# Optimization experiments

Measured on AMD Instinct MI355X. Metric: run time of the kernel, lower is better.

Reference implementation:

```python
import jax, jax.numpy as jnp
import numpy as np

H = 768          # hidden_size
HH = H // 2      # 384


def setup_inputs() -> dict:
    key = jax.random.key(0)
    ks = jax.random.split(key, 16)
    B, W, E, R = 32, 512, 128, 1024
    inp = {
        "hidden_states": jax.random.normal(ks[0], (B, W, H), dtype=jnp.float32),
        "relation_head": jax.random.randint(ks[1], (B, R), 0, E),
        "relation_tail": jax.random.randint(ks[2], (B, R), 0, E),
        "relation_label": jax.random.randint(ks[3], (B, R), 0, 2),
        "entities_start": jax.random.randint(ks[4], (B, E), 0, W),
        "entities_end": jax.random.randint(ks[5], (B, E), 0, W),
        "entities_label": jax.random.randint(ks[6], (B, E), 0, 3),
        # parameters (torch Linear convention: weight [out, in])
        "entity_emb": jax.random.normal(ks[7], (3, H), dtype=jnp.float32) * 0.02,
        "Wh1": jax.random.normal(ks[8], (H, 2 * H), dtype=jnp.float32) * 0.02,
        "bh1": jnp.zeros((H,), jnp.float32),
        "Wh2": jax.random.normal(ks[9], (HH, H), dtype=jnp.float32) * 0.02,
        "bh2": jnp.zeros((HH,), jnp.float32),
        "Wt1": jax.random.normal(ks[10], (H, 2 * H), dtype=jnp.float32) * 0.02,
        "bt1": jnp.zeros((H,), jnp.float32),
        "Wt2": jax.random.normal(ks[11], (HH, H), dtype=jnp.float32) * 0.02,
        "bt2": jnp.zeros((HH,), jnp.float32),
        "W_bil": jax.random.normal(ks[12], (2, HH, HH), dtype=jnp.float32) * 0.02,
        "W_lin": jax.random.normal(ks[13], (2, 2 * HH), dtype=jnp.float32) * 0.02,
        "b_lin": jnp.zeros((2,), jnp.float32),
    }
    return inp


def _ffnn(x, W1, b1, W2, b2):
    # two-layer MLP with ReLU (dropout is identity in eval mode)
    h = jax.nn.relu(jnp.einsum('brd,hd->brh', x, W1) + b1)
    return jax.nn.relu(jnp.einsum('brh,oh->bro', h, W2) + b2)


def reference(hidden_states, relation_head, relation_tail, relation_label,
              entities_start, entities_end, entities_label,
              entity_emb, Wh1, bh1, Wh2, bh2, Wt1, bt1, Wt2, bt2,
              W_bil, W_lin, b_lin):
    # gather per-relation entity info: [B, R]
    head_index = jnp.take_along_axis(entities_start, relation_head, axis=1)
    head_label = jnp.take_along_axis(entities_label, relation_head, axis=1)
    tail_index = jnp.take_along_axis(entities_start, relation_tail, axis=1)
    tail_label = jnp.take_along_axis(entities_label, relation_tail, axis=1)

    # gather token reprs: [B, R, H]
    head_tok = jnp.take_along_axis(hidden_states, head_index[:, :, None], axis=1)
    tail_tok = jnp.take_along_axis(hidden_states, tail_index[:, :, None], axis=1)

    head_repr = jnp.concatenate([head_tok, entity_emb[head_label]], axis=-1)  # [B,R,2H]
    tail_repr = jnp.concatenate([tail_tok, entity_emb[tail_label]], axis=-1)

    heads = _ffnn(head_repr, Wh1, bh1, Wh2, bh2)  # [B,R,HH]
    tails = _ffnn(tail_repr, Wt1, bt1, Wt2, bt2)

    # biaffine: bilinear + linear on concat
    bil = jnp.einsum('bri,oij,brj->bro', heads, W_bil, tails)
    lin = jnp.einsum('brc,oc->bro', jnp.concatenate([heads, tails], axis=-1), W_lin) + b_lin
    logits = bil + lin  # [B, R, 2]

    # per-doc mean CE summed over docs
    logp = jax.nn.log_softmax(logits, axis=-1)
    nll = -jnp.take_along_axis(logp, relation_label[:, :, None], axis=-1)[..., 0]  # [B,R]
    loss = jnp.sum(jnp.mean(nll, axis=1))
    return loss
```

## Files before the change

### kernel.cpp

```cpp
#include <hip/hip_runtime.h>
#include <math.h>

typedef unsigned short u16;
typedef __bf16 bf16x8 __attribute__((ext_vector_type(8)));
typedef float f32x4 __attribute__((ext_vector_type(4)));

#define B_ 32
#define W_ 512
#define H_ 768
#define HH_ 384
#define E_ 128
#define R_ 1024
#define BE_ (B_*E_)
#define K1_ (2*H_)
#define BKK 64

__device__ __forceinline__ u16 f2bf(float f) {
  unsigned u = __float_as_uint(f);
  u = (u + 0x7fffu + ((u >> 16) & 1u)) >> 16;
  return (u16)u;
}
__device__ __forceinline__ float bf2f(u16 u) {
  return __uint_as_float(((unsigned)u) << 16);
}

__device__ __forceinline__ void gload_lds16(const void* g, void* l) {
  __builtin_amdgcn_global_load_lds(
      (__attribute__((address_space(1))) void*)(g),
      (__attribute__((address_space(3))) void*)(l), 16, 0, 0);
}

__device__ __forceinline__ void xcd_swizzle(int& bx, int& by) {
  const int nwg = gridDim.x * gridDim.y;
  int orig = blockIdx.y * gridDim.x + blockIdx.x;
  int q = nwg >> 3, r = nwg & 7;
  int xcd = orig & 7, idx = orig >> 3;
  int wgid = (xcd < r ? xcd * (q + 1) : r * (q + 1) + (xcd - r) * q) + idx;
  bx = wgid % gridDim.x;
  by = wgid / gridDim.x;
}

#define NBLK_W 2017
#define NBLK_P 1152
#define NBLK_X 4096

__global__ __launch_bounds__(256) void prep_all(
    const float* __restrict__ Wh1, const float* __restrict__ Wt1,
    const float* __restrict__ Wh2, const float* __restrict__ Wt2,
    const float* __restrict__ Wbil,
    const float* __restrict__ bh1, const float* __restrict__ bt1,
    const float* __restrict__ bh2, const float* __restrict__ bt2,
    const float* __restrict__ emb,
    const float* __restrict__ hs, const int* __restrict__ ent_start,
    u16* __restrict__ W1c, u16* __restrict__ W2c, u16* __restrict__ Wb,
    float* __restrict__ b2cat, float* __restrict__ P, u16* __restrict__ X)
{
  const int blk = blockIdx.x;
  const int tid = threadIdx.x;

  if (blk < NBLK_W) {
    const int i = blk * 256 + tid;
    const int SW1 = 294912;
    const int SW2 = SW1 + 147456;
    const int SWB = SW2 + 73728;
    const int SB2 = SWB + 192;
    if (i < SW1) {
      int row = i / 192, c = i % 192;
      const float4* src = (const float4*)((row < 768)
          ? (Wh1 + (size_t)row * K1_) : (Wt1 + (size_t)(row - 768) * K1_));
      float4 v = src[c];
      ushort4 o; o.x = f2bf(v.x); o.y = f2bf(v.y); o.z = f2bf(v.z); o.w = f2bf(v.w);
      ((ushort4*)W1c)[i] = o;
    } else if (i < SW2) {
      int j = i - SW1;
      float4 v = (j < 73728) ? ((const float4*)Wh2)[j]
                             : ((const float4*)Wt2)[j - 73728];
      ushort4 o; o.x = f2bf(v.x); o.y = f2bf(v.y); o.z = f2bf(v.z); o.w = f2bf(v.w);
      ((ushort4*)W2c)[j] = o;
    } else if (i < SWB) {
      int j = i - SW2;
      float4 v = ((const float4*)Wbil)[j];
      ushort4 o; o.x = f2bf(v.x); o.y = f2bf(v.y); o.z = f2bf(v.z); o.w = f2bf(v.w);
      ((ushort4*)Wb)[j] = o;
    } else if (i < SB2) {
      int j = i - SWB;
      ((float4*)b2cat)[j] = (j < 96) ? ((const float4*)bh2)[j]
                                     : ((const float4*)bt2)[j - 96];
    }
  } else if (blk < NBLK_W + NBLK_P) {
    const int w = (blk - NBLK_W) * 4 + (tid >> 6);
    const int lane = tid & 63;
    const int l = w / K1_;
    const int n = w - l * K1_;
    const float* wrow = (n < 768) ? (Wh1 + (size_t)n * K1_ + 768)
                                  : (Wt1 + (size_t)(n - 768) * K1_ + 768);
    const float  bb   = (n < 768) ? bh1[n] : bt1[n - 768];
    const float* ev = emb + (size_t)l * H_;
    float s = 0.f;
#pragma unroll
    for (int t = 0; t < 12; ++t) {
      int d = lane + 64 * t;
      s += ev[d] * wrow[d];
    }
#pragma unroll
    for (int off = 32; off; off >>= 1) s += __shfl_down(s, off);
    if (lane == 0) P[(size_t)l * K1_ + n] = s + bb;
  } else {
    const int be = blk - (NBLK_W + NBLK_P);
    if (tid < 192) {
      int b = be >> 7;
      int start = ent_start[be];
      const float4* s0 = (const float4*)(hs + ((size_t)b * W_ + start) * H_);
      float4 v = s0[tid];
      ushort4 o; o.x = f2bf(v.x); o.y = f2bf(v.y); o.z = f2bf(v.z); o.w = f2bf(v.w);
      ((ushort4*)(X + (size_t)be * H_))[tid] = o;
    }
  }
}

#define BM 128
#define BN 128

__global__ __launch_bounds__(256, 2) void gemm_bf16(
    const u16* __restrict__ A, int lda,
    const u16* __restrict__ Wt,
    const float* __restrict__ bias,
    u16* __restrict__ C, int ldc,
    int M, int N, int K, int do_relu, int half_n, int aoff,
    const float* __restrict__ rowBias,
    const int* __restrict__ rowLabel, int ldP)
{
  __shared__ char smem[2 * 32768];

  int bx, by;
  xcd_swizzle(bx, by);
  const int bn = bx * BN;
  const int bm = by * BM;

  const int tid  = threadIdx.x;
  const int wid  = tid >> 6;
  const int lane = tid & 63;
  const int wm = ((wid >> 1) & 1) * 64;
  const int wn = (wid & 1) * 64;

  const int a0 = (half_n && bn >= half_n) ? aoff : 0;

  const int srow = lane >> 3;
  const int sk8  = (lane & 7) ^ srow;
  const u16* gA = A  + (size_t)(bm + 32*wid + srow) * lda + a0 + 8*sk8;
  const u16* gB = Wt + (size_t)(bn + 32*wid + srow) * K  + 8*sk8;

  const int frow = lane & 15;
  const int fk8  = lane >> 4;

  f32x4 acc[4][4] = {};

  auto stage = [&](int buf, int k0) {
    char* As = smem + buf * 32768;
    char* Bs = As + 16384;
#pragma unroll
    for (int i = 0; i < 4; ++i) {
      gload_lds16(gA + k0 + (size_t)i * 8 * lda, As + (4*wid + i) * 1024);
      gload_lds16(gB + k0 + (size_t)i * 8 * K,   Bs + (4*wid + i) * 1024);
    }
  };

  const int nt = K / BKK;
  stage(0, 0);

  for (int t = 0; t < nt; ++t) {
    const int cur = t & 1;
    if (t + 1 < nt) {
      stage(cur ^ 1, (t + 1) * BKK);
      asm volatile("s_waitcnt vmcnt(8)" ::: "memory");
    } else {
      asm volatile("s_waitcnt vmcnt(0)" ::: "memory");
    }
    __builtin_amdgcn_s_barrier();

    char* As = smem + cur * 32768;
    char* Bs = As + 16384;
#pragma unroll
    for (int kh = 0; kh < 2; ++kh) {
      bf16x8 a[4], b[4];
#pragma unroll
      for (int m = 0; m < 4; ++m) {
        const int row  = wm + m*16 + frow;
        const int slot = (kh*4 + fk8) ^ (row & 7);
        a[m] = *(const bf16x8*)(As + row*128 + slot*16);
      }
#pragma unroll
      for (int n = 0; n < 4; ++n) {
        const int row  = wn + n*16 + frow;
        const int slot = (kh*4 + fk8) ^ (row & 7);
        b[n] = *(const bf16x8*)(Bs + row*128 + slot*16);
      }
#pragma unroll
      for (int m = 0; m < 4; ++m)
#pragma unroll
        for (int n = 0; n < 4; ++n)
          acc[m][n] = __builtin_amdgcn_mfma_f32_16x16x32_bf16(
              a[m], b[n], acc[m][n], 0, 0, 0);
    }

    if (t + 1 < nt)
      __builtin_amdgcn_s_barrier();
  }

  int lbl[4][4];
  if (rowLabel) {
#pragma unroll
    for (int m = 0; m < 4; ++m)
#pragma unroll
      for (int r = 0; r < 4; ++r)
        lbl[m][r] = rowLabel[bm + wm + m*16 + fk8*4 + r];
  }

#pragma unroll
  for (int n = 0; n < 4; ++n) {
    const int col = bn + wn + n*16 + frow;
    const float bv = bias ? bias[col] : 0.f;
    float p0 = 0.f, p1 = 0.f, p2 = 0.f;
    if (rowLabel) {
      p0 = rowBias[col];
      p1 = rowBias[ldP + col];
      p2 = rowBias[2*ldP + col];
    }
#pragma unroll
    for (int m = 0; m < 4; ++m) {
#pragma unroll
      for (int r = 0; r < 4; ++r) {
        const int row = bm + wm + m*16 + fk8*4 + r;
        float v = acc[m][n][r] + bv;
        if (rowLabel) {
          int l = lbl[m][r];
          v += (l == 0) ? p0 : ((l == 1) ? p1 : p2);
        }
        if (do_relu) v = fmaxf(v, 0.f);
        C[(size_t)row * ldc + col] = f2bf(v);
      }
    }
  }
}

__global__ __launch_bounds__(256, 2) void gemm_S_ce(
    const u16* __restrict__ Hcat, const u16* __restrict__ U,
    const float* __restrict__ linHT, const float* __restrict__ b_lin,
    const int* __restrict__ rel_head, const int* __restrict__ rel_tail,
    const int* __restrict__ rel_label, float* __restrict__ out)
{
  __shared__ char smem[2 * 16384];
  __shared__ float Sl[64][65];
  __shared__ float red[4];

  const int xcd = blockIdx.x & 7, idx = blockIdx.x >> 3;
  const int wgid = xcd * 32 + idx;
  const int bn = (wgid & 3) * 64;
  const int zz = wgid >> 2;
  const int z  = zz >> 1;
  const int bm = (zz & 1) * 64;

  const int tid  = threadIdx.x;
  const int wid  = tid >> 6;
  const int lane = tid & 63;
  const int srow = lane >> 3;
  const int sk8  = (lane & 7) ^ srow;

  auto stage = [&](int buf, int k0) {
    char* base = smem + buf * 16384;
#pragma unroll
    for (int i = 0; i < 4; ++i) {
      const int u = wid * 4 + i;
      if (u < 8) {
        const int row = z*128 + bm + u*8 + srow;
        gload_lds16(Hcat + (size_t)row * 768 + k0 + 8*sk8, base + u*1024);
      } else {
        const int row = bn + (u - 8)*8 + srow;
        gload_lds16(U + (size_t)z*98304 + (size_t)row * 384 + k0 + 8*sk8,
                    base + u*1024);
      }
    }
  };

  const int wm = (wid >> 1) * 32;
  const int wn = (wid & 1) * 32;
  const int frow = lane & 15;
  const int fk8  = lane >> 4;

  f32x4 acc[2][2] = {};

  stage(0, 0);

  for (int t = 0; t < 6; ++t) {
    const int cur = t & 1;
    if (t + 1 < 6) {
      stage(cur ^ 1, (t + 1) * BKK);
      asm volatile("s_waitcnt vmcnt(4)" ::: "memory");
    } else {
      asm volatile("s_waitcnt vmcnt(0)" ::: "memory");
    }
    __builtin_amdgcn_s_barrier();

    char* As = smem + cur * 16384;
    char* Bs = As + 8192;
#pragma unroll
    for (int kh = 0; kh < 2; ++kh) {
      bf16x8 a[2], b[2];
#pragma unroll
      for (int m = 0; m < 2; ++m) {
        const int row  = wm + m*16 + frow;
        const int slot = (kh*4 + fk8) ^ (row & 7);
        a[m] = *(const bf16x8*)(As + row*128 + slot*16);
      }
#pragma unroll
      for (int n = 0; n < 2; ++n) {
        const int row  = wn + n*16 + frow;
        const int slot = (kh*4 + fk8) ^ (row & 7);
        b[n] = *(const bf16x8*)(Bs + row*128 + slot*16);
      }
#pragma unroll
      for (int m = 0; m < 2; ++m)
#pragma unroll
        for (int n = 0; n < 2; ++n)
          acc[m][n] = __builtin_amdgcn_mfma_f32_16x16x32_bf16(
              a[m], b[n], acc[m][n], 0, 0, 0);
    }

    if (t + 1 < 6)
      __builtin_amdgcn_s_barrier();
  }

  const int o = frow & 1;
  const float blv = b_lin[o];
#pragma unroll
  for (int n = 0; n < 2; ++n) {
    const int lc = wn + n*16 + frow;
    const int e2 = (bn + lc) >> 1;
    const float lt = linHT[(size_t)(z*128 + e2) * 4 + 2 + o];
#pragma unroll
    for (int m = 0; m < 2; ++m) {
#pragma unroll
      for (int r = 0; r < 4; ++r) {
        const int lr = wm + m*16 + fk8*4 + r;
        const float lh = linHT[(size_t)(z*128 + bm + lr) * 4 + o];
        Sl[lr][lc] = acc[m][n][r] + lh + lt + blv;
      }
    }
  }
  __syncthreads();

  float nllsum = 0.f;
#pragma unroll
  for (int j = 0; j < 4; ++j) {
    const int i = z * 1024 + tid + 256 * j;
    const int rh = rel_head[i];
    const int rt = rel_tail[i];
    const int lab = rel_label[i];
    if ((unsigned)(rh - bm) < 64u && (unsigned)(rt*2 - bn) < 64u) {
      const float l0 = Sl[rh - bm][rt*2 - bn];
      const float l1 = Sl[rh - bm][rt*2 - bn + 1];
      const float mx = fmaxf(l0, l1);
      const float lse = mx + logf(expf(l0 - mx) + expf(l1 - mx));
      nllsum += lse - (lab == 0 ? l0 : l1);
    }
  }
#pragma unroll
  for (int off = 32; off; off >>= 1) nllsum += __shfl_down(nllsum, off);
  if (lane == 0) red[wid] = nllsum;
  __syncthreads();
  if (tid == 0)
    atomicAdd(out, (red[0] + red[1] + red[2] + red[3]) * (1.0f / R_));
}

__global__ __launch_bounds__(256) void lin_parts_kernel(
    const u16* __restrict__ Hcat, const float* __restrict__ W_lin,
    float* __restrict__ linHT, float* __restrict__ out)
{
  if (blockIdx.x == 0 && threadIdx.x == 0) out[0] = 0.f;
  const int wave = blockIdx.x * 4 + (threadIdx.x >> 6);
  const int lane = threadIdx.x & 63;
  const int nwave = gridDim.x * 4;

  for (int be = wave; be < BE_; be += nwave) {
    const ushort4* src = (const ushort4*)(Hcat + (size_t)be * 768);
    float s0 = 0.f, s1 = 0.f, s2 = 0.f, s3 = 0.f;
#pragma unroll
    for (int rd = 0; rd < 3; ++rd) {
      const int idx4 = rd * 64 + lane;
      const int c = idx4 * 4;
      ushort4 v4 = src[idx4];
      float4 w0 = *(const float4*)(W_lin + c);
      float4 w1 = *(const float4*)(W_lin + 768 + c);
      float d0 = bf2f(v4.x)*w0.x + bf2f(v4.y)*w0.y + bf2f(v4.z)*w0.z + bf2f(v4.w)*w0.w;
      float d1 = bf2f(v4.x)*w1.x + bf2f(v4.y)*w1.y + bf2f(v4.z)*w1.z + bf2f(v4.w)*w1.w;
      if (c < 384) { s0 += d0; s1 += d1; }
      else         { s2 += d0; s3 += d1; }
    }
#pragma unroll
    for (int off = 32; off; off >>= 1) {
      s0 += __shfl_down(s0, off);
      s1 += __shfl_down(s1, off);
      s2 += __shfl_down(s2, off);
      s3 += __shfl_down(s3, off);
    }
    if (lane == 0) {
      float4 v = {s0, s1, s2, s3};
      *(float4*)(linHT + (size_t)be * 4) = v;
    }
  }
}

extern "C" void kernel_launch(void* const* d_in, const int* in_sizes, int n_in,
                              void* d_out, int out_size, void* d_ws, size_t ws_size,
                              hipStream_t stream)
{
  const float* hs        = (const float*)d_in[0];
  const int*   rel_head  = (const int*)  d_in[1];
  const int*   rel_tail  = (const int*)  d_in[2];
  const int*   rel_label = (const int*)  d_in[3];
  const int*   ent_start = (const int*)  d_in[4];
  const int*   ent_label = (const int*)  d_in[6];
  const float* emb   = (const float*)d_in[7];
  const float* Wh1   = (const float*)d_in[8];
  const float* bh1   = (const float*)d_in[9];
  const float* Wh2   = (const float*)d_in[10];
  const float* bh2   = (const float*)d_in[11];
  const float* Wt1   = (const float*)d_in[12];
  const float* bt1   = (const float*)d_in[13];
  const float* Wt2   = (const float*)d_in[14];
  const float* bt2   = (const float*)d_in[15];
  const float* W_bil = (const float*)d_in[16];
  const float* W_lin = (const float*)d_in[17];
  const float* b_lin = (const float*)d_in[18];
  float* out = (float*)d_out;

  u16* X    = (u16*)d_ws;
  u16* H1   = X    + (size_t)BE_ * H_;
  u16* Hcat = H1   + (size_t)BE_ * K1_;
  u16* U    = Hcat + (size_t)BE_ * H_;
  u16* W1c  = U    + (size_t)BE_ * H_;
  u16* W2c  = W1c  + (size_t)K1_ * H_;
  u16* Wb   = W2c  + (size_t)H_ * H_;
  float* b2cat = (float*)(Wb + (size_t)H_ * HH_);
  float* P     = b2cat + H_;
  float* linHT = P + 3*K1_;

  prep_all<<<dim3(NBLK_W + NBLK_P + NBLK_X), dim3(256), 0, stream>>>(
      Wh1, Wt1, Wh2, Wt2, W_bil, bh1, bt1, bh2, bt2, emb,
      hs, ent_start, W1c, W2c, Wb, b2cat, P, X);

  gemm_bf16<<<dim3(K1_/BN, BE_/BM), dim3(256), 0, stream>>>(
      X, H_, W1c, (const float*)nullptr, H1, K1_, BE_, K1_, H_, 1, 0, 0,
      P, ent_label, K1_);

  gemm_bf16<<<dim3(H_/BN, BE_/BM), dim3(256), 0, stream>>>(
      H1, K1_, W2c, b2cat, Hcat, H_, BE_, H_, H_, 1, HH_, H_,
      (const float*)nullptr, (const int*)nullptr, 0);

  lin_parts_kernel<<<dim3(128), dim3(256), 0, stream>>>(Hcat, W_lin, linHT, out);

  gemm_bf16<<<dim3(H_/BN, BE_/BM), dim3(256), 0, stream>>>(
      Hcat + HH_, H_, Wb, (const float*)nullptr, U, H_, BE_, H_, HH_, 0, 0, 0,
      (const float*)nullptr, (const int*)nullptr, 0);

  gemm_S_ce<<<dim3(256), dim3(256), 0, stream>>>(
      Hcat, U, linHT, b_lin, rel_head, rel_tail, rel_label, out);
}
```

Baseline: 68.39 us.

## Fold W2/Wbil conversion and linear-part kernel into GEMM launches as tail blocks

The W2, bilinear weight and second-layer bias bf16 conversions move out of the prep kernel and into extra tail blocks of the first GEMM launch. The separate lin_parts kernel is removed and its work runs as tail blocks appended to the bilinear GEMM launch. This cuts one kernel launch and overlaps small memory-bound work with GEMM tiles. In exchange the GEMM kernel takes many more parameters, and the XCD swizzle is recomputed over only the GEMM block count.

```diff
diff --git a/kernel.cpp b/kernel.cpp
--- a/kernel.cpp
+++ b/kernel.cpp
@@ -11,8 +11,8 @@
 #define HH_ 384
 #define E_ 128
 #define R_ 1024
-#define BE_ (B_*E_)
-#define K1_ (2*H_)
+#define BE_ 4096
+#define K1_ 1536
 #define BKK 64
 
 __device__ __forceinline__ u16 f2bf(float f) {
@@ -23,78 +23,42 @@
 __device__ __forceinline__ float bf2f(u16 u) {
   return __uint_as_float(((unsigned)u) << 16);
 }
-
 __device__ __forceinline__ void gload_lds16(const void* g, void* l) {
   __builtin_amdgcn_global_load_lds(
       (__attribute__((address_space(1))) void*)(g),
       (__attribute__((address_space(3))) void*)(l), 16, 0, 0);
 }
 
-__device__ __forceinline__ void xcd_swizzle(int& bx, int& by) {
-  const int nwg = gridDim.x * gridDim.y;
-  int orig = blockIdx.y * gridDim.x + blockIdx.x;
-  int q = nwg >> 3, r = nwg & 7;
-  int xcd = orig & 7, idx = orig >> 3;
-  int wgid = (xcd < r ? xcd * (q + 1) : r * (q + 1) + (xcd - r) * q) + idx;
-  bx = wgid % gridDim.x;
-  by = wgid / gridDim.x;
-}
-
-#define NBLK_W 2017
-#define NBLK_P 1152
-#define NBLK_X 4096
+#define NBLK_W1 1152
+#define NBLK_P  1152
+#define NBLK_X  4096
 
 __global__ __launch_bounds__(256) void prep_all(
     const float* __restrict__ Wh1, const float* __restrict__ Wt1,
-    const float* __restrict__ Wh2, const float* __restrict__ Wt2,
-    const float* __restrict__ Wbil,
     const float* __restrict__ bh1, const float* __restrict__ bt1,
-    const float* __restrict__ bh2, const float* __restrict__ bt2,
     const float* __restrict__ emb,
     const float* __restrict__ hs, const int* __restrict__ ent_start,
-    u16* __restrict__ W1c, u16* __restrict__ W2c, u16* __restrict__ Wb,
-    float* __restrict__ b2cat, float* __restrict__ P, u16* __restrict__ X)
+    u16* __restrict__ W1c, float* __restrict__ P, u16* __restrict__ X)
 {
   const int blk = blockIdx.x;
   const int tid = threadIdx.x;
 
-  if (blk < NBLK_W) {
+  if (blk < NBLK_W1) {
     const int i = blk * 256 + tid;
-    const int SW1 = 294912;
-    const int SW2 = SW1 + 147456;
-    const int SWB = SW2 + 73728;
-    const int SB2 = SWB + 192;
-    if (i < SW1) {
-      int row = i / 192, c = i % 192;
-      const float4* src = (const float4*)((row < 768)
-          ? (Wh1 + (size_t)row * K1_) : (Wt1 + (size_t)(row - 768) * K1_));
-      float4 v = src[c];
-      ushort4 o; o.x = f2bf(v.x); o.y = f2bf(v.y); o.z = f2bf(v.z); o.w = f2bf(v.w);
-      ((ushort4*)W1c)[i] = o;
-    } else if (i < SW2) {
-      int j = i - SW1;
-      float4 v = (j < 73728) ? ((const float4*)Wh2)[j]
-                             : ((const float4*)Wt2)[j - 73728];
-      ushort4 o; o.x = f2bf(v.x); o.y = f2bf(v.y); o.z = f2bf(v.z); o.w = f2bf(v.w);
-      ((ushort4*)W2c)[j] = o;
-    } else if (i < SWB) {
-      int j = i - SW2;
-      float4 v = ((const float4*)Wbil)[j];
-      ushort4 o; o.x = f2bf(v.x); o.y = f2bf(v.y); o.z = f2bf(v.z); o.w = f2bf(v.w);
-      ((ushort4*)Wb)[j] = o;
-    } else if (i < SB2) {
-      int j = i - SWB;
-      ((float4*)b2cat)[j] = (j < 96) ? ((const float4*)bh2)[j]
-                                     : ((const float4*)bt2)[j - 96];
-    }
-  } else if (blk < NBLK_W + NBLK_P) {
-    const int w = (blk - NBLK_W) * 4 + (tid >> 6);
+    int row = i / 192, c = i % 192;
+    const float4* src = (const float4*)((row < 768)
+        ? (Wh1 + (size_t)row * K1_) : (Wt1 + (size_t)(row - 768) * K1_));
+    float4 v = src[c];
+    ushort4 o; o.x = f2bf(v.x); o.y = f2bf(v.y); o.z = f2bf(v.z); o.w = f2bf(v.w);
+    ((ushort4*)W1c)[i] = o;
+  } else if (blk < NBLK_W1 + NBLK_P) {
+    const int w = (blk - NBLK_W1) * 4 + (tid >> 6);
     const int lane = tid & 63;
     const int l = w / K1_;
     const int n = w - l * K1_;
     const float* wrow = (n < 768) ? (Wh1 + (size_t)n * K1_ + 768)
                                   : (Wt1 + (size_t)(n - 768) * K1_ + 768);
-    const float  bb   = (n < 768) ? bh1[n] : bt1[n - 768];
+    const float bb = (n < 768) ? bh1[n] : bt1[n - 768];
     const float* ev = emb + (size_t)l * H_;
     float s = 0.f;
 #pragma unroll
@@ -106,12 +70,11 @@
     for (int off = 32; off; off >>= 1) s += __shfl_down(s, off);
     if (lane == 0) P[(size_t)l * K1_ + n] = s + bb;
   } else {
-    const int be = blk - (NBLK_W + NBLK_P);
+    const int be = blk - (NBLK_W1 + NBLK_P);
     if (tid < 192) {
       int b = be >> 7;
       int start = ent_start[be];
-      const float4* s0 = (const float4*)(hs + ((size_t)b * W_ + start) * H_);
-      float4 v = s0[tid];
+      float4 v = ((const float4*)(hs + ((size_t)b * W_ + start) * H_))[tid];
       ushort4 o; o.x = f2bf(v.x); o.y = f2bf(v.y); o.z = f2bf(v.z); o.w = f2bf(v.w);
       ((ushort4*)(X + (size_t)be * H_))[tid] = o;
     }
@@ -126,18 +89,85 @@
     const u16* __restrict__ Wt,
     const float* __restrict__ bias,
     u16* __restrict__ C, int ldc,
-    int M, int N, int K, int do_relu, int half_n, int aoff,
+    int K, int do_relu, int half_n, int aoff,
     const float* __restrict__ rowBias,
-    const int* __restrict__ rowLabel, int ldP)
+    const int* __restrict__ rowLabel, int ldP,
+    int ngemm,
+    const float* __restrict__ tWh2, const float* __restrict__ tWt2,
+    const float* __restrict__ tWbil,
+    const float* __restrict__ tbh2, const float* __restrict__ tbt2,
+    u16* __restrict__ tW2c, u16* __restrict__ tWb, float* __restrict__ tb2cat,
+    const u16* __restrict__ linSrc, const float* __restrict__ W_lin,
+    float* __restrict__ linHT, float* __restrict__ outZ)
 {
   __shared__ char smem[2 * 32768];
 
-  int bx, by;
-  xcd_swizzle(bx, by);
-  const int bn = bx * BN;
-  const int bm = by * BM;
-
   const int tid  = threadIdx.x;
+  const int id   = blockIdx.y * gridDim.x + blockIdx.x;
+
+  if (id >= ngemm) {
+    const int tailid = id - ngemm;
+    const int ntail  = gridDim.x * gridDim.y - ngemm;
+    if (tW2c) {
+      for (int i = tailid * 256 + tid; i < 221376; i += ntail * 256) {
+        if (i < 147456) {
+          float4 v = (i < 73728) ? ((const float4*)tWh2)[i]
+                                 : ((const float4*)tWt2)[i - 73728];
+          ushort4 o; o.x = f2bf(v.x); o.y = f2bf(v.y); o.z = f2bf(v.z); o.w = f2bf(v.w);
+          ((ushort4*)tW2c)[i] = o;
+        } else if (i < 221184) {
+          int j = i - 147456;
+          float4 v = ((const float4*)tWbil)[j];
+          ushort4 o; o.x = f2bf(v.x); o.y = f2bf(v.y); o.z = f2bf(v.z); o.w = f2bf(v.w);
+          ((ushort4*)tWb)[j] = o;
+        } else {
+          int j = i - 221184;
+          ((float4*)tb2cat)[j] = (j < 96) ? ((const float4*)tbh2)[j]
+                                          : ((const float4*)tbt2)[j - 96];
+        }
+      }
+    } else if (linHT) {
+      if (tailid == 0 && tid == 0) outZ[0] = 0.f;
+      const int wave  = tailid * 4 + (tid >> 6);
+      const int nwave = ntail * 4;
+      const int lane  = tid & 63;
+      for (int be = wave; be < BE_; be += nwave) {
+        const ushort4* src = (const ushort4*)(linSrc + (size_t)be * 768);
+        float s0 = 0.f, s1 = 0.f, s2 = 0.f, s3 = 0.f;
+#pragma unroll
+        for (int rd = 0; rd < 3; ++rd) {
+          const int idx4 = rd * 64 + lane;
+          const int c = idx4 * 4;
+          ushort4 v4 = src[idx4];
+          float4 w0 = *(const float4*)(W_lin + c);
+          float4 w1 = *(const float4*)(W_lin + 768 + c);
+          float d0 = bf2f(v4.x)*w0.x + bf2f(v4.y)*w0.y + bf2f(v4.z)*w0.z + bf2f(v4.w)*w0.w;
+          float d1 = bf2f(v4.x)*w1.x + bf2f(v4.y)*w1.y + bf2f(v4.z)*w1.z + bf2f(v4.w)*w1.w;
+          if (c < 384) { s0 += d0; s1 += d1; }
+          else         { s2 += d0; s3 += d1; }
+        }
+#pragma unroll
+        for (int off = 32; off; off >>= 1) {
+          s0 += __shfl_down(s0, off);
+          s1 += __shfl_down(s1, off);
+          s2 += __shfl_down(s2, off);
+          s3 += __shfl_down(s3, off);
+        }
+        if (lane == 0) {
+          float4 v = {s0, s1, s2, s3};
+          *(float4*)(linHT + (size_t)be * 4) = v;
+        }
+      }
+    }
+    return;
+  }
+
+  const int q = ngemm >> 3, r = ngemm & 7;
+  const int xcd = id & 7, idx = id >> 3;
+  const int wgid = (xcd < r ? xcd * (q + 1) : r * (q + 1) + (xcd - r) * q) + idx;
+  const int bn = (wgid % gridDim.x) * BN;
+  const int bm = (wgid / gridDim.x) * BM;
+
   const int wid  = tid >> 6;
   const int lane = tid & 63;
   const int wm = ((wid >> 1) & 1) * 64;
@@ -370,44 +400,6 @@
   __syncthreads();
   if (tid == 0)
     atomicAdd(out, (red[0] + red[1] + red[2] + red[3]) * (1.0f / R_));
-}
-
-__global__ __launch_bounds__(256) void lin_parts_kernel(
-    const u16* __restrict__ Hcat, const float* __restrict__ W_lin,
-    float* __restrict__ linHT, float* __restrict__ out)
-{
-  if (blockIdx.x == 0 && threadIdx.x == 0) out[0] = 0.f;
-  const int wave = blockIdx.x * 4 + (threadIdx.x >> 6);
-  const int lane = threadIdx.x & 63;
-  const int nwave = gridDim.x * 4;
-
-  for (int be = wave; be < BE_; be += nwave) {
-    const ushort4* src = (const ushort4*)(Hcat + (size_t)be * 768);
-    float s0 = 0.f, s1 = 0.f, s2 = 0.f, s3 = 0.f;
-#pragma unroll
-    for (int rd = 0; rd < 3; ++rd) {
-      const int idx4 = rd * 64 + lane;
-      const int c = idx4 * 4;
-      ushort4 v4 = src[idx4];
-      float4 w0 = *(const float4*)(W_lin + c);
-      float4 w1 = *(const float4*)(W_lin + 768 + c);
-      float d0 = bf2f(v4.x)*w0.x + bf2f(v4.y)*w0.y + bf2f(v4.z)*w0.z + bf2f(v4.w)*w0.w;
-      float d1 = bf2f(v4.x)*w1.x + bf2f(v4.y)*w1.y + bf2f(v4.z)*w1.z + bf2f(v4.w)*w1.w;
-      if (c < 384) { s0 += d0; s1 += d1; }
-      else         { s2 += d0; s3 += d1; }
-    }
-#pragma unroll
-    for (int off = 32; off; off >>= 1) {
-      s0 += __shfl_down(s0, off);
-      s1 += __shfl_down(s1, off);
-      s2 += __shfl_down(s2, off);
-      s3 += __shfl_down(s3, off);
-    }
-    if (lane == 0) {
-      float4 v = {s0, s1, s2, s3};
-      *(float4*)(linHT + (size_t)be * 4) = v;
-    }
-  }
 }
 
 extern "C" void kernel_launch(void* const* d_in, const int* in_sizes, int n_in,
@@ -429,7 +421,7 @@
   const float* bt1   = (const float*)d_in[13];
   const float* Wt2   = (const float*)d_in[14];
   const float* bt2   = (const float*)d_in[15];
-  const float* W_bil = (const float*)d_in[16];
+  const float* Wbil  = (const float*)d_in[16];
   const float* W_lin = (const float*)d_in[17];
   const float* b_lin = (const float*)d_in[18];
   float* out = (float*)d_out;
@@ -445,23 +437,30 @@
   float* P     = b2cat + H_;
   float* linHT = P + 3*K1_;
 
-  prep_all<<<dim3(NBLK_W + NBLK_P + NBLK_X), dim3(256), 0, stream>>>(
-      Wh1, Wt1, Wh2, Wt2, W_bil, bh1, bt1, bh2, bt2, emb,
-      hs, ent_start, W1c, W2c, Wb, b2cat, P, X);
-
-  gemm_bf16<<<dim3(K1_/BN, BE_/BM), dim3(256), 0, stream>>>(
-      X, H_, W1c, (const float*)nullptr, H1, K1_, BE_, K1_, H_, 1, 0, 0,
-      P, ent_label, K1_);
-
-  gemm_bf16<<<dim3(H_/BN, BE_/BM), dim3(256), 0, stream>>>(
-      H1, K1_, W2c, b2cat, Hcat, H_, BE_, H_, H_, 1, HH_, H_,
-      (const float*)nullptr, (const int*)nullptr, 0);
-
-  lin_parts_kernel<<<dim3(128), dim3(256), 0, stream>>>(Hcat, W_lin, linHT, out);
-
-  gemm_bf16<<<dim3(H_/BN, BE_/BM), dim3(256), 0, stream>>>(
-      Hcat + HH_, H_, Wb, (const float*)nullptr, U, H_, BE_, H_, HH_, 0, 0, 0,
-      (const float*)nullptr, (const int*)nullptr, 0);
+  prep_all<<<dim3(NBLK_W1 + NBLK_P + NBLK_X), dim3(256), 0, stream>>>(
+      Wh1, Wt1, bh1, bt1, emb, hs, ent_start, W1c, P, X);
+
+  gemm_bf16<<<dim3(12, 34), dim3(256), 0, stream>>>(
+      X, H_, W1c, (const float*)nullptr, H1, K1_, H_, 1, 0, 0,
+      P, ent_label, K1_, 384,
+      Wh2, Wt2, Wbil, bh2, bt2, W2c, Wb, b2cat,
+      (const u16*)nullptr, (const float*)nullptr, (float*)nullptr, (float*)nullptr);
+
+  gemm_bf16<<<dim3(6, 32), dim3(256), 0, stream>>>(
+      H1, K1_, W2c, b2cat, Hcat, H_, H_, 1, HH_, H_,
+      (const float*)nullptr, (const int*)nullptr, 0, 192,
+      (const float*)nullptr, (const float*)nullptr, (const float*)nullptr,
+      (const float*)nullptr, (const float*)nullptr,
+      (u16*)nullptr, (u16*)nullptr, (float*)nullptr,
+      (const u16*)nullptr, (const float*)nullptr, (float*)nullptr, (float*)nullptr);
+
+  gemm_bf16<<<dim3(6, 54), dim3(256), 0, stream>>>(
+      Hcat + HH_, H_, Wb, (const float*)nullptr, U, H_, HH_, 0, 0, 0,
+      (const float*)nullptr, (const int*)nullptr, 0, 192,
+      (const float*)nullptr, (const float*)nullptr, (const float*)nullptr,
+      (const float*)nullptr, (const float*)nullptr,
+      (u16*)nullptr, (u16*)nullptr, (float*)nullptr,
+      Hcat, W_lin, linHT, out);
 
   gemm_S_ce<<<dim3(256), dim3(256), 0, stream>>>(
       Hcat, U, linHT, b_lin, rel_head, rel_tail, rel_label, out);
```

New measurement: 62.98 us. -7.9%, faster.
